# Kernel tuning notes

Measured on AMD Instinct MI355X. Metric: run time of the kernel, lower is better.

Reference implementation:

```python
import jax, jax.numpy as jnp
import numpy as np

N = 100000   # nodes
F_IN = 128   # node features
H = 32       # hidden size (hard-coded in module)


def setup_inputs() -> dict:
    key = jax.random.key(0)
    ks = jax.random.split(key, 20)
    inp = {
        'x': jax.random.normal(ks[0], (N, F_IN), dtype=jnp.float32),
        'edge_index': jax.random.randint(ks[1], (2, 3200000), 0, N, dtype=jnp.int64),
        'edge_weight': jax.random.uniform(ks[2], (3200000,), dtype=jnp.float32),
        'prev_hidden_state': jax.random.normal(ks[3], (N, H), dtype=jnp.float32),
    }
    s = 1.0 / np.sqrt(F_IN)
    s2 = 1.0 / np.sqrt(2 * H)
    sh = 1.0 / np.sqrt(H)
    # GCNConv weights (in->H) + bias, for gates z, r, h
    for i, g in enumerate(['z', 'r', 'h']):
        inp[f'Wc_{g}'] = jax.random.uniform(ks[4 + i], (F_IN, H), minval=-s, maxval=s, dtype=jnp.float32)
        inp[f'bc_{g}'] = jnp.zeros((H,), dtype=jnp.float32)
        # torch Linear(2H -> H): weight [H, 2H], bias [H]
        inp[f'Wl_{g}'] = jax.random.uniform(ks[8 + i], (H, 2 * H), minval=-s2, maxval=s2, dtype=jnp.float32)
        inp[f'bl_{g}'] = jax.random.uniform(ks[12 + i], (H,), minval=-s2, maxval=s2, dtype=jnp.float32)
    inp['W_head'] = jax.random.uniform(ks[16], (1, H), minval=-sh, maxval=sh, dtype=jnp.float32)
    inp['b_head'] = jax.random.uniform(ks[17], (1,), minval=-sh, maxval=sh, dtype=jnp.float32)
    return inp


def _gcn_norm(edge_index, edge_weight):
    # add self-loops with weight 1, symmetric GCN normalization
    loop = jnp.arange(N, dtype=edge_index.dtype)
    row = jnp.concatenate([edge_index[0], loop])
    col = jnp.concatenate([edge_index[1], loop])
    w = jnp.concatenate([edge_weight, jnp.ones((N,), dtype=edge_weight.dtype)])
    deg = jax.ops.segment_sum(w, col, num_segments=N)
    dinv = jnp.where(deg > 0, jax.lax.rsqrt(jnp.where(deg > 0, deg, 1.0)), 0.0)
    norm = dinv[row] * w * dinv[col]
    return row, col, norm


def _gcn_conv(x, W, b, row, col, norm):
    xw = x @ W                                   # [N, H]
    agg = jax.ops.segment_sum(norm[:, None] * xw[row], col, num_segments=N)
    return agg + b


def reference(x, edge_index, edge_weight, prev_hidden_state,
              Wc_z, bc_z, Wl_z, bl_z,
              Wc_r, bc_r, Wl_r, bl_r,
              Wc_h, bc_h, Wl_h, bl_h,
              W_head, b_head):
    row, col, norm = _gcn_norm(edge_index, edge_weight)
    Hprev = prev_hidden_state

    cz = _gcn_conv(x, Wc_z, bc_z, row, col, norm)
    Z = jax.nn.sigmoid(jnp.concatenate([cz, Hprev], axis=1) @ Wl_z.T + bl_z)

    cr = _gcn_conv(x, Wc_r, bc_r, row, col, norm)
    R = jax.nn.sigmoid(jnp.concatenate([cr, Hprev], axis=1) @ Wl_r.T + bl_r)

    ch = _gcn_conv(x, Wc_h, bc_h, row, col, norm)
    Ht = jnp.tanh(jnp.concatenate([ch, Hprev * R], axis=1) @ Wl_h.T + bl_h)

    Hnew = Z * Hprev + (1.0 - Z) * Ht
    y = jax.nn.relu(Hnew) @ W_head.T + b_head    # [N, 1]
    return (y, Hnew)
```

## Files before the change

### kernel.cpp

```cpp
#include <hip/hip_runtime.h>

#define NN 100000
#define FIN 128
#define HD 32
#define EE 3200000
#define NBUK 391
#define EPB 6144
#define NBLK ((EE + EPB - 1) / EPB)
#define CAP 10240

typedef unsigned int uint;
typedef unsigned short ushort;
typedef float vfloat4 __attribute__((ext_vector_type(4)));

__device__ __forceinline__ ushort f2bf(float f) {
    uint b = __float_as_uint(f);
    return (ushort)((b + 0x7FFFu + ((b >> 16) & 1u)) >> 16);
}

__device__ __forceinline__ int load_idx32_c(const int* __restrict__ ei, long long pos, int is64) {
    return is64 ? ei[pos * 2] : ei[pos];
}
__device__ __forceinline__ int load_idx32_nt(const int* __restrict__ ei, long long pos, int is64) {
    return is64 ? __builtin_nontemporal_load(ei + pos * 2)
                : __builtin_nontemporal_load(ei + pos);
}

__global__ void zero_gcur(int* __restrict__ gcur) {
    for (int i = threadIdx.x; i < 6400; i += 512) gcur[i] = 0;
}

__global__ __launch_bounds__(512) void sortC_fused(const int* __restrict__ ei,
                                                   const float* __restrict__ wt,
                                                   int* __restrict__ gcur,
                                                   uint2* __restrict__ erec2) {
    __shared__ uint2 lrec[EPB];
    __shared__ int hist[NBUK];
    __shared__ int lbase[NBUK];
    __shared__ int lcombo[NBUK];
    __shared__ int lcur[NBUK];
    __shared__ int sis64;
    int tid = threadIdx.x, blk = blockIdx.x;
    for (int b = tid; b < NBUK; b += 512) hist[b] = 0;
    if (tid < 64) {
        uint v = 0;
#pragma unroll
        for (int r = 0; r < 4; r++) v |= ((const uint*)ei)[2 * (tid + 64 * r) + 1];
        unsigned long long nz = __ballot(v != 0u);
        if (tid == 0) sis64 = (nz == 0ULL) ? 1 : 0;
    }
    __syncthreads();
    int is64 = sis64;
    int e0 = blk * EPB, e1 = e0 + EPB; if (e1 > EE) e1 = EE;
    for (int e = e0 + tid; e < e1; e += 512) {
        int col = load_idx32_c(ei, (long long)EE + e, is64);
        atomicAdd(&hist[col >> 8], 1);
    }
    __syncthreads();
    for (int b = tid; b < NBUK; b += 512)
        lbase[b] = hist[b] ? atomicAdd(&gcur[b * 16], hist[b]) : 0;
    __syncthreads();
    if (tid < 64) {
        int run = 0;
        for (int c = 0; c < NBUK; c += 64) {
            int b = c + tid;
            int v = (b < NBUK) ? hist[b] : 0;
            int incl = v;
#pragma unroll
            for (int d = 1; d < 64; d <<= 1) {
                int t2 = __shfl_up(incl, d, 64);
                if (tid >= d) incl += t2;
            }
            if (b < NBUK) {
                int ls = run + incl - v;
                lcur[b] = ls;
                lcombo[b] = b * CAP + lbase[b] - ls;
            }
            run += __shfl(incl, 63, 64);
        }
    }
    __syncthreads();
    for (int e = e0 + tid; e < e1; e += 512) {
        int row = load_idx32_nt(ei, e, is64);
        int col = load_idx32_c(ei, (long long)EE + e, is64);
        uint nb = __float_as_uint(__builtin_nontemporal_load(wt + e));
        uint enc = ((nb + 0x8000u) >> 16) & 0x7FFFu;
        int pos = atomicAdd(&lcur[col >> 8], 1);
        uint2 r; r.x = (uint)row | (enc << 17); r.y = (uint)col;
        lrec[pos] = r;
    }
    __syncthreads();
    int m = e1 - e0;
    for (int slot = tid; slot < m; slot += 512) {
        uint2 r = lrec[slot];
        erec2[lcombo[r.y >> 8] + slot] = r;
    }
}

__global__ __launch_bounds__(512) void passB_fine(const uint2* __restrict__ erec2,
                                                  const int* __restrict__ gcur,
                                                  uint* __restrict__ erecF,
                                                  int* __restrict__ estart, int* __restrict__ cnt,
                                                  float* __restrict__ dinv) {
    __shared__ int hist[256];
    __shared__ float wsum[256];
    __shared__ int off[256];
    __shared__ int cur[256];
    __shared__ int sd[256];
    int t = threadIdx.x, b = blockIdx.x;
    if (t < 256) { hist[t] = 0; wsum[t] = 0.f; }
    __syncthreads();
    int e0 = b * CAP, e1 = e0 + gcur[b * 16];
    for (int e = e0 + t; e < e1; e += 512) {
        uint2 r = erec2[e];
        int cl = (int)(r.y & 255u);
        atomicAdd(&hist[cl], 1);
        atomicAdd(&wsum[cl], __uint_as_float((r.x >> 17) << 16));
    }
    __syncthreads();
    int v = 0;
    if (t < 256) { v = hist[t]; sd[t] = v; }
    __syncthreads();
    for (int o = 1; o < 256; o <<= 1) {
        int x = (t >= o && t < 256) ? sd[t - o] : 0;
        __syncthreads();
        if (t < 256) sd[t] += x;
        __syncthreads();
    }
    if (t < 256) {
        off[t] = sd[t] - v;
        cur[t] = 0;
        int node = b * 256 + t;
        if (node < NN) {
            estart[node] = e0 + off[t];
            cnt[node] = v;
            dinv[node] = rsqrtf(1.0f + wsum[t]);
        }
    }
    __syncthreads();
    for (int e = e0 + t; e < e1; e += 512) {
        uint2 r = erec2[e];
        int cl = (int)(r.y & 255u);
        int p = atomicAdd(&cur[cl], 1);
        erecF[e0 + off[cl] + p] = r.x;
    }
}

__global__ __launch_bounds__(256) void gemm_xw_kernel(
        const float* __restrict__ x,
        const float* __restrict__ Wz, const float* __restrict__ Wr, const float* __restrict__ Wh,
        const float* __restrict__ dinv,
        ushort* __restrict__ xw16) {
    __shared__ float Bs[128 * 96];
    __shared__ float AsT[8 * 128];
    int tid = threadIdx.x;
    int tx = tid & 31, ty = tid >> 5;
    int rowBase = blockIdx.x * 128;

    for (int e = tid; e < 4096; e += 256) { int k = e >> 5, c = e & 31; Bs[k * 96 + c]      = Wz[e]; }
    for (int e = tid; e < 4096; e += 256) { int k = e >> 5, c = e & 31; Bs[k * 96 + 32 + c] = Wr[e]; }
    for (int e = tid; e < 4096; e += 256) { int k = e >> 5, c = e & 31; Bs[k * 96 + 64 + c] = Wh[e]; }

    float acc0[16], acc1[16], acc2[16];
#pragma unroll
    for (int r = 0; r < 16; r++) { acc0[r] = 0.f; acc1[r] = 0.f; acc2[r] = 0.f; }

    int lr = tid >> 1;
    int lc = (tid & 1) * 4;
    for (int k0 = 0; k0 < 128; k0 += 8) {
        __syncthreads();
        int gr = rowBase + lr;
        vfloat4 a4 = (vfloat4)(0.f);
        if (gr < NN) a4 = __builtin_nontemporal_load((const vfloat4*)(x + (long long)gr * FIN + k0 + lc));
        AsT[(lc + 0) * 128 + lr] = a4.x;
        AsT[(lc + 1) * 128 + lr] = a4.y;
        AsT[(lc + 2) * 128 + lr] = a4.z;
        AsT[(lc + 3) * 128 + lr] = a4.w;
        __syncthreads();
#pragma unroll
        for (int kk = 0; kk < 8; kk++) {
            float b0 = Bs[(k0 + kk) * 96 + tx];
            float b1 = Bs[(k0 + kk) * 96 + 32 + tx];
            float b2 = Bs[(k0 + kk) * 96 + 64 + tx];
            const float4* ap = (const float4*)(AsT + kk * 128 + ty * 16);
            float4 a0 = ap[0], a1 = ap[1], a2 = ap[2], a3 = ap[3];
            float av[16] = {a0.x,a0.y,a0.z,a0.w, a1.x,a1.y,a1.z,a1.w,
                            a2.x,a2.y,a2.z,a2.w, a3.x,a3.y,a3.z,a3.w};
#pragma unroll
            for (int r = 0; r < 16; r++) {
                acc0[r] = fmaf(av[r], b0, acc0[r]);
                acc1[r] = fmaf(av[r], b1, acc1[r]);
                acc2[r] = fmaf(av[r], b2, acc2[r]);
            }
        }
    }
#pragma unroll
    for (int r = 0; r < 16; r++) {
        int gr = rowBase + ty * 16 + r;
        if (gr < NN) {
            float di = dinv[gr];
            ushort* o = xw16 + (long long)gr * 128;
            uint w0 = (uint)f2bf(acc0[r] * di) | ((uint)f2bf(acc1[r] * di) << 16);
            uint w1 = (uint)f2bf(acc2[r] * di);
            uint2 pk; pk.x = w0; pk.y = w1;
            *(uint2*)(o + 4 * tx) = pk;
        }
    }
}

__global__ __launch_bounds__(512) void agg_gate_kernel(
        const uint* __restrict__ erecF, const int* __restrict__ estart, const int* __restrict__ cnt,
        const ushort* __restrict__ xw16, const float* __restrict__ dinv,
        const float* __restrict__ hprev,
        const float* __restrict__ bcz, const float* __restrict__ bcr, const float* __restrict__ bch,
        const float* __restrict__ Wlz, const float* __restrict__ blz,
        const float* __restrict__ Wlr, const float* __restrict__ blr,
        const float* __restrict__ Wlh, const float* __restrict__ blh,
        const float* __restrict__ Whead, const float* __restrict__ bhead,
        float* __restrict__ y, float* __restrict__ hnew) {
    __shared__ float WzT[64 * 32], WrT[64 * 32], WhT[64 * 32];
    __shared__ float czs[16][32], crs[16][32], chs[16][32], hps[16][32], rhs[16][32];
    __shared__ uint rwsh[16][32];
    int tid = threadIdx.x;
    for (int e2 = tid; e2 < 2048; e2 += 512) {
        int jj = e2 >> 6, k = e2 & 63;
        WzT[k * 32 + jj] = Wlz[e2];
        WrT[k * 32 + jj] = Wlr[e2];
        WhT[k * 32 + jj] = Wlh[e2];
    }
    int s = tid >> 5, j = tid & 31;
    int i = blockIdx.x * 16 + s;
    int beg = estart[i], c = cnt[i], end = beg + c;

    const char* xwb = (const char*)xw16;
    uint jo8 = 8u * (uint)j;

    float cz = 0.f, cr = 0.f, ch = 0.f;
    int e = beg + j;
    uint vcur = (e < end) ? __builtin_nontemporal_load(erecF + e) : 0u;
    __syncthreads();

#define REC(vv, dd)                                                        \
    {                                                                      \
        float w_ = __uint_as_float(((vv) >> 17) << 16);                    \
        cz = fmaf(w_, __uint_as_float((dd).x << 16), cz);                  \
        cr = fmaf(w_, __uint_as_float((dd).x & 0xFFFF0000u), cr);          \
        ch = fmaf(w_, __uint_as_float((dd).y << 16), ch);                  \
    }

    for (int base = beg; base < end; base += 32) {
        rwsh[s][j] = vcur;
        int en = base + 32 + j;
        uint vnext = (en < end) ? __builtin_nontemporal_load(erecF + en) : 0u;
        int mm = end - base; if (mm > 32) mm = 32;
        int t = 0;
        for (; t + 8 <= mm; t += 8) {
            uint v0 = rwsh[s][t + 0], v1 = rwsh[s][t + 1], v2 = rwsh[s][t + 2], v3 = rwsh[s][t + 3];
            uint v4 = rwsh[s][t + 4], v5 = rwsh[s][t + 5], v6 = rwsh[s][t + 6], v7 = rwsh[s][t + 7];
            uint b0 = (v0 & 0x1FFFFu) * 256u, b1 = (v1 & 0x1FFFFu) * 256u;
            uint b2 = (v2 & 0x1FFFFu) * 256u, b3 = (v3 & 0x1FFFFu) * 256u;
            uint b4 = (v4 & 0x1FFFFu) * 256u, b5 = (v5 & 0x1FFFFu) * 256u;
            uint b6 = (v6 & 0x1FFFFu) * 256u, b7 = (v7 & 0x1FFFFu) * 256u;
            uint2 d0 = *(const uint2*)(xwb + b0 + jo8);
            uint2 d1 = *(const uint2*)(xwb + b1 + jo8);
            uint2 d2 = *(const uint2*)(xwb + b2 + jo8);
            uint2 d3 = *(const uint2*)(xwb + b3 + jo8);
            uint2 d4 = *(const uint2*)(xwb + b4 + jo8);
            uint2 d5 = *(const uint2*)(xwb + b5 + jo8);
            uint2 d6 = *(const uint2*)(xwb + b6 + jo8);
            uint2 d7 = *(const uint2*)(xwb + b7 + jo8);
            REC(v0, d0) REC(v1, d1) REC(v2, d2) REC(v3, d3)
            REC(v4, d4) REC(v5, d5) REC(v6, d6) REC(v7, d7)
        }
        for (; t + 4 <= mm; t += 4) {
            uint v0 = rwsh[s][t + 0], v1 = rwsh[s][t + 1], v2 = rwsh[s][t + 2], v3 = rwsh[s][t + 3];
            uint b0 = (v0 & 0x1FFFFu) * 256u, b1 = (v1 & 0x1FFFFu) * 256u;
            uint b2 = (v2 & 0x1FFFFu) * 256u, b3 = (v3 & 0x1FFFFu) * 256u;
            uint2 d0 = *(const uint2*)(xwb + b0 + jo8);
            uint2 d1 = *(const uint2*)(xwb + b1 + jo8);
            uint2 d2 = *(const uint2*)(xwb + b2 + jo8);
            uint2 d3 = *(const uint2*)(xwb + b3 + jo8);
            REC(v0, d0) REC(v1, d1) REC(v2, d2) REC(v3, d3)
        }
        for (; t < mm; t++) {
            uint v0 = rwsh[s][t];
            uint b0 = (v0 & 0x1FFFFu) * 256u;
            uint2 d0 = *(const uint2*)(xwb + b0 + jo8);
            REC(v0, d0)
        }
        vcur = vnext;
    }
#undef REC

    float di = dinv[i];
    uint2 dself = *(const uint2*)(xwb + (uint)i * 256u + jo8);
    czs[s][j] = fmaf(di, cz + __uint_as_float(dself.x << 16), bcz[j]);
    crs[s][j] = fmaf(di, cr + __uint_as_float(dself.x & 0xFFFF0000u), bcr[j]);
    chs[s][j] = fmaf(di, ch + __uint_as_float(dself.y << 16), bch[j]);
    float hp = hprev[(long long)i * HD + j];
    hps[s][j] = hp;
    __syncthreads();

    float az = blz[j], arv = blr[j];
#pragma unroll
    for (int k = 0; k < 32; k++) {
        az  = fmaf(WzT[k * 32 + j], czs[s][k], az);
        arv = fmaf(WrT[k * 32 + j], crs[s][k], arv);
    }
#pragma unroll
    for (int k = 0; k < 32; k++) {
        float v = hps[s][k];
        az  = fmaf(WzT[(k + 32) * 32 + j], v, az);
        arv = fmaf(WrT[(k + 32) * 32 + j], v, arv);
    }
    float Z = 1.f / (1.f + __expf(-az));
    float R = 1.f / (1.f + __expf(-arv));
    rhs[s][j] = hp * R;
    __syncthreads();

    float ah = blh[j];
#pragma unroll
    for (int k = 0; k < 32; k++) ah = fmaf(WhT[k * 32 + j], chs[s][k], ah);
#pragma unroll
    for (int k = 0; k < 32; k++) ah = fmaf(WhT[(k + 32) * 32 + j], rhs[s][k], ah);
    float Ht = tanhf(ah);
    float hn = Z * hp + (1.f - Z) * Ht;
    float yv = fmaxf(hn, 0.f) * Whead[j];
#pragma unroll
    for (int m = 16; m; m >>= 1) yv += __shfl_xor(yv, m, 32);
    hnew[(long long)i * HD + j] = hn;
    if (j == 0) y[i] = yv + bhead[0];
}

extern "C" void kernel_launch(void* const* d_in, const int* in_sizes, int n_in,
                              void* d_out, int out_size, void* d_ws, size_t ws_size,
                              hipStream_t stream) {
    const float* x     = (const float*)d_in[0];
    const int*   ei    = (const int*)d_in[1];
    const float* wt    = (const float*)d_in[2];
    const float* hprev = (const float*)d_in[3];
    const float* Wcz = (const float*)d_in[4],  *bcz = (const float*)d_in[5];
    const float* Wlz = (const float*)d_in[6],  *blz = (const float*)d_in[7];
    const float* Wcr = (const float*)d_in[8],  *bcr = (const float*)d_in[9];
    const float* Wlr = (const float*)d_in[10], *blr = (const float*)d_in[11];
    const float* Wch = (const float*)d_in[12], *bch = (const float*)d_in[13];
    const float* Wlh = (const float*)d_in[14], *blh = (const float*)d_in[15];
    const float* Whead = (const float*)d_in[16], *bhead = (const float*)d_in[17];

    float* out_y = (float*)d_out;
    float* out_h = (float*)d_out + NN;

    float* ws = (float*)d_ws;
    float* dinv      = ws;
    int*   estart    = (int*)(ws + NN);
    int*   cnt       = (int*)(ws + 2LL * NN);
    int*   gcur      = (int*)(ws + 3LL * NN);
    uint2* erec2     = (uint2*)(ws + 3LL * NN + 6400);
    ushort* xw16     = (ushort*)erec2;
    uint*  erecF     = (uint*)(ws + 3LL * NN + 6400 + 2LL * NBUK * CAP);

    zero_gcur<<<1, 512, 0, stream>>>(gcur);
    sortC_fused<<<NBLK, 512, 0, stream>>>(ei, wt, gcur, erec2);
    passB_fine<<<NBUK, 512, 0, stream>>>(erec2, gcur, erecF, estart, cnt, dinv);
    gemm_xw_kernel<<<(NN + 127) / 128, 256, 0, stream>>>(x, Wcz, Wcr, Wch, dinv, xw16);
    agg_gate_kernel<<<NN / 16, 512, 0, stream>>>(
        erecF, estart, cnt, xw16, dinv, hprev, bcz, bcr, bch,
        Wlz, blz, Wlr, blr, Wlh, blh, Whead, bhead, out_y, out_h);
}
```

Measured before the change: 423.6 us.

## Replace two-pass bucket sort with per-node fixed-capacity slab scatter

```diff
diff --git a/kernel.cpp b/kernel.cpp
--- a/kernel.cpp
+++ b/kernel.cpp
@@ -4,10 +4,7 @@
 #define FIN 128
 #define HD 32
 #define EE 3200000
-#define NBUK 391
-#define EPB 6144
-#define NBLK ((EE + EPB - 1) / EPB)
-#define CAP 10240
+#define SLAB 84
 
 typedef unsigned int uint;
 typedef unsigned short ushort;
@@ -18,30 +15,22 @@
     return (ushort)((b + 0x7FFFu + ((b >> 16) & 1u)) >> 16);
 }
 
-__device__ __forceinline__ int load_idx32_c(const int* __restrict__ ei, long long pos, int is64) {
-    return is64 ? ei[pos * 2] : ei[pos];
-}
 __device__ __forceinline__ int load_idx32_nt(const int* __restrict__ ei, long long pos, int is64) {
     return is64 ? __builtin_nontemporal_load(ei + pos * 2)
                 : __builtin_nontemporal_load(ei + pos);
 }
 
-__global__ void zero_gcur(int* __restrict__ gcur) {
-    for (int i = threadIdx.x; i < 6400; i += 512) gcur[i] = 0;
-}
-
-__global__ __launch_bounds__(512) void sortC_fused(const int* __restrict__ ei,
-                                                   const float* __restrict__ wt,
-                                                   int* __restrict__ gcur,
-                                                   uint2* __restrict__ erec2) {
-    __shared__ uint2 lrec[EPB];
-    __shared__ int hist[NBUK];
-    __shared__ int lbase[NBUK];
-    __shared__ int lcombo[NBUK];
-    __shared__ int lcur[NBUK];
+__global__ __launch_bounds__(512) void zero_ncur(int* __restrict__ ncur) {
+    int i = blockIdx.x * 512 + threadIdx.x;
+    if (i < NN) ncur[i] = 0;
+}
+
+__global__ __launch_bounds__(512) void scatter_kernel(const int* __restrict__ ei,
+                                                      const float* __restrict__ wt,
+                                                      int* __restrict__ ncur,
+                                                      uint* __restrict__ erecF) {
     __shared__ int sis64;
-    int tid = threadIdx.x, blk = blockIdx.x;
-    for (int b = tid; b < NBUK; b += 512) hist[b] = 0;
+    int tid = threadIdx.x;
     if (tid < 64) {
         uint v = 0;
 #pragma unroll
@@ -51,99 +40,34 @@
     }
     __syncthreads();
     int is64 = sis64;
-    int e0 = blk * EPB, e1 = e0 + EPB; if (e1 > EE) e1 = EE;
-    for (int e = e0 + tid; e < e1; e += 512) {
-        int col = load_idx32_c(ei, (long long)EE + e, is64);
-        atomicAdd(&hist[col >> 8], 1);
-    }
-    __syncthreads();
-    for (int b = tid; b < NBUK; b += 512)
-        lbase[b] = hist[b] ? atomicAdd(&gcur[b * 16], hist[b]) : 0;
-    __syncthreads();
-    if (tid < 64) {
-        int run = 0;
-        for (int c = 0; c < NBUK; c += 64) {
-            int b = c + tid;
-            int v = (b < NBUK) ? hist[b] : 0;
-            int incl = v;
-#pragma unroll
-            for (int d = 1; d < 64; d <<= 1) {
-                int t2 = __shfl_up(incl, d, 64);
-                if (tid >= d) incl += t2;
-            }
-            if (b < NBUK) {
-                int ls = run + incl - v;
-                lcur[b] = ls;
-                lcombo[b] = b * CAP + lbase[b] - ls;
-            }
-            run += __shfl(incl, 63, 64);
-        }
-    }
-    __syncthreads();
-    for (int e = e0 + tid; e < e1; e += 512) {
+    int stride = gridDim.x * 512;
+    for (int e = blockIdx.x * 512 + tid; e < EE; e += stride) {
         int row = load_idx32_nt(ei, e, is64);
-        int col = load_idx32_c(ei, (long long)EE + e, is64);
+        int col = load_idx32_nt(ei, (long long)EE + e, is64);
         uint nb = __float_as_uint(__builtin_nontemporal_load(wt + e));
         uint enc = ((nb + 0x8000u) >> 16) & 0x7FFFu;
-        int pos = atomicAdd(&lcur[col >> 8], 1);
-        uint2 r; r.x = (uint)row | (enc << 17); r.y = (uint)col;
-        lrec[pos] = r;
-    }
-    __syncthreads();
-    int m = e1 - e0;
-    for (int slot = tid; slot < m; slot += 512) {
-        uint2 r = lrec[slot];
-        erec2[lcombo[r.y >> 8] + slot] = r;
-    }
-}
-
-__global__ __launch_bounds__(512) void passB_fine(const uint2* __restrict__ erec2,
-                                                  const int* __restrict__ gcur,
-                                                  uint* __restrict__ erecF,
-                                                  int* __restrict__ estart, int* __restrict__ cnt,
-                                                  float* __restrict__ dinv) {
-    __shared__ int hist[256];
-    __shared__ float wsum[256];
-    __shared__ int off[256];
-    __shared__ int cur[256];
-    __shared__ int sd[256];
-    int t = threadIdx.x, b = blockIdx.x;
-    if (t < 256) { hist[t] = 0; wsum[t] = 0.f; }
-    __syncthreads();
-    int e0 = b * CAP, e1 = e0 + gcur[b * 16];
-    for (int e = e0 + t; e < e1; e += 512) {
-        uint2 r = erec2[e];
-        int cl = (int)(r.y & 255u);
-        atomicAdd(&hist[cl], 1);
-        atomicAdd(&wsum[cl], __uint_as_float((r.x >> 17) << 16));
-    }
-    __syncthreads();
-    int v = 0;
-    if (t < 256) { v = hist[t]; sd[t] = v; }
-    __syncthreads();
-    for (int o = 1; o < 256; o <<= 1) {
-        int x = (t >= o && t < 256) ? sd[t - o] : 0;
-        __syncthreads();
-        if (t < 256) sd[t] += x;
-        __syncthreads();
-    }
-    if (t < 256) {
-        off[t] = sd[t] - v;
-        cur[t] = 0;
-        int node = b * 256 + t;
-        if (node < NN) {
-            estart[node] = e0 + off[t];
-            cnt[node] = v;
-            dinv[node] = rsqrtf(1.0f + wsum[t]);
-        }
-    }
-    __syncthreads();
-    for (int e = e0 + t; e < e1; e += 512) {
-        uint2 r = erec2[e];
-        int cl = (int)(r.y & 255u);
-        int p = atomicAdd(&cur[cl], 1);
-        erecF[e0 + off[cl] + p] = r.x;
-    }
+        int pos = atomicAdd(&ncur[col], 1);
+        erecF[col * SLAB + pos] = (uint)row | (enc << 17);
+    }
+}
+
+__global__ __launch_bounds__(256) void dinv_kernel(const uint* __restrict__ erecF,
+                                                   const int* __restrict__ ncur,
+                                                   float* __restrict__ dinv) {
+    int i = blockIdx.x * 256 + threadIdx.x;
+    if (i >= NN) return;
+    const uint* p = erecF + i * SLAB;
+    int c = ncur[i];
+    float s0 = 0.f, s1 = 0.f, s2 = 0.f, s3 = 0.f;
+    int k = 0;
+    for (; k + 4 <= c; k += 4) {
+        s0 += __uint_as_float((p[k + 0] >> 17) << 16);
+        s1 += __uint_as_float((p[k + 1] >> 17) << 16);
+        s2 += __uint_as_float((p[k + 2] >> 17) << 16);
+        s3 += __uint_as_float((p[k + 3] >> 17) << 16);
+    }
+    for (; k < c; k++) s0 += __uint_as_float((p[k] >> 17) << 16);
+    dinv[i] = rsqrtf(1.0f + ((s0 + s1) + (s2 + s3)));
 }
 
 __global__ __launch_bounds__(256) void gemm_xw_kernel(
@@ -209,7 +133,7 @@
 }
 
 __global__ __launch_bounds__(512) void agg_gate_kernel(
-        const uint* __restrict__ erecF, const int* __restrict__ estart, const int* __restrict__ cnt,
+        const uint* __restrict__ erecF, const int* __restrict__ cnt,
         const ushort* __restrict__ xw16, const float* __restrict__ dinv,
         const float* __restrict__ hprev,
         const float* __restrict__ bcz, const float* __restrict__ bcr, const float* __restrict__ bch,
@@ -230,7 +154,7 @@
     }
     int s = tid >> 5, j = tid & 31;
     int i = blockIdx.x * 16 + s;
-    int beg = estart[i], c = cnt[i], end = beg + c;
+    int beg = i * SLAB, c = cnt[i], end = beg + c;
 
     const char* xwb = (const char*)xw16;
     uint jo8 = 8u * (uint)j;
@@ -351,19 +275,16 @@
     float* out_h = (float*)d_out + NN;
 
     float* ws = (float*)d_ws;
-    float* dinv      = ws;
-    int*   estart    = (int*)(ws + NN);
-    int*   cnt       = (int*)(ws + 2LL * NN);
-    int*   gcur      = (int*)(ws + 3LL * NN);
-    uint2* erec2     = (uint2*)(ws + 3LL * NN + 6400);
-    ushort* xw16     = (ushort*)erec2;
-    uint*  erecF     = (uint*)(ws + 3LL * NN + 6400 + 2LL * NBUK * CAP);
-
-    zero_gcur<<<1, 512, 0, stream>>>(gcur);
-    sortC_fused<<<NBLK, 512, 0, stream>>>(ei, wt, gcur, erec2);
-    passB_fine<<<NBUK, 512, 0, stream>>>(erec2, gcur, erecF, estart, cnt, dinv);
+    int*   ncur  = (int*)ws;
+    float* dinv  = ws + NN;
+    uint*  erecF = (uint*)(ws + 2LL * NN);
+    ushort* xw16 = (ushort*)(ws + 2LL * NN + (long long)NN * SLAB);
+
+    zero_ncur<<<(NN + 511) / 512, 512, 0, stream>>>(ncur);
+    scatter_kernel<<<1024, 512, 0, stream>>>(ei, wt, ncur, erecF);
+    dinv_kernel<<<(NN + 255) / 256, 256, 0, stream>>>(erecF, ncur, dinv);
     gemm_xw_kernel<<<(NN + 127) / 128, 256, 0, stream>>>(x, Wcz, Wcr, Wch, dinv, xw16);
     agg_gate_kernel<<<NN / 16, 512, 0, stream>>>(
-        erecF, estart, cnt, xw16, dinv, hprev, bcz, bcr, bch,
+        erecF, ncur, xw16, dinv, hprev, bcz, bcr, bch,
         Wlz, blz, Wlr, blr, Wlh, blh, Whead, bhead, out_y, out_h);
 }
```

Result: slower. 497.8 us (+17.5%).
